# Optimization experiments

Hardware: AMD Instinct MI355X
Metric: run time of the kernel (lower is better)

## Reference

```python
import jax, jax.numpy as jnp
import numpy as np

NEG_SLOPE = 0.2  # PyG GATConv default LeakyReLU slope


def gat_layer(x, src, dst, W, a_src, a_dst, bias, num_nodes, heads, out_ch, concat):
    # x: [N, in], W: [in, heads*out_ch], a_src/a_dst: [heads, out_ch]
    h = (x @ W).reshape(num_nodes, heads, out_ch)          # [N,H,C]
    alpha_s = jnp.sum(h * a_src, axis=-1)                  # [N,H]
    alpha_d = jnp.sum(h * a_dst, axis=-1)                  # [N,H]
    e = jax.nn.leaky_relu(alpha_s[src] + alpha_d[dst], NEG_SLOPE)  # [E,H]
    # softmax over incoming edges of each destination node
    e_max = jax.ops.segment_max(e, dst, num_segments=num_nodes)   # [N,H]
    e_exp = jnp.exp(e - e_max[dst])                        # [E,H]
    denom = jax.ops.segment_sum(e_exp, dst, num_segments=num_nodes)  # [N,H]
    alpha = e_exp / denom[dst]                             # [E,H]
    msg = h[src] * alpha[:, :, None]                       # [E,H,C]
    out = jax.ops.segment_sum(msg, dst, num_segments=num_nodes)     # [N,H,C]
    if concat:
        out = out.reshape(num_nodes, heads * out_ch)
    else:
        out = out.mean(axis=1)
    return out + bias


def setup_inputs() -> dict:
    key = jax.random.key(0)
    ks = jax.random.split(key, 12)
    N, E = 50000, 800000
    IN, HID, OUT, H = 128, 32, 64, 4
    x = jax.random.normal(ks[0], (N, IN), dtype=jnp.float32)
    edge_index = jax.random.randint(ks[1], (2, E), 0, N, dtype=jnp.int32)
    s = 1.0 / np.sqrt(IN)
    W1 = jax.random.normal(ks[2], (IN, H * HID), dtype=jnp.float32) * s
    a_src1 = jax.random.normal(ks[3], (H, HID), dtype=jnp.float32) * 0.1
    a_dst1 = jax.random.normal(ks[4], (H, HID), dtype=jnp.float32) * 0.1
    b1 = jnp.zeros((H * HID,), dtype=jnp.float32)
    s2 = 1.0 / np.sqrt(H * HID)
    W2 = jax.random.normal(ks[5], (H * HID, OUT), dtype=jnp.float32) * s2
    a_src2 = jax.random.normal(ks[6], (1, OUT), dtype=jnp.float32) * 0.1
    a_dst2 = jax.random.normal(ks[7], (1, OUT), dtype=jnp.float32) * 0.1
    b2 = jnp.zeros((OUT,), dtype=jnp.float32)
    return {"x": x, "edge_index": edge_index, "W1": W1, "a_src1": a_src1,
            "a_dst1": a_dst1, "b1": b1, "W2": W2, "a_src2": a_src2,
            "a_dst2": a_dst2, "b2": b2}


def reference(x, edge_index, W1, a_src1, a_dst1, b1, W2, a_src2, a_dst2, b2):
    N = x.shape[0]
    src, dst = edge_index[0], edge_index[1]
    h = gat_layer(x, src, dst, W1, a_src1, a_dst1, b1, N, heads=4, out_ch=32, concat=True)
    h = jax.nn.elu(h)
    # dropout is identity in eval / p=0.0
    out = gat_layer(h, src, dst, W2, a_src2, a_dst2, b2, N, heads=1, out_ch=64, concat=False)
    return out
```

## Files before the change

### kernel.cpp

```cpp
#include <hip/hip_runtime.h>
#include <hip/hip_bf16.h>

#define C1 128
#define C2 64
#define CAP 96

typedef __attribute__((ext_vector_type(8))) short short8;
typedef __attribute__((ext_vector_type(4))) float floatx4;

__device__ __forceinline__ float lrelu(float v) { return v > 0.f ? v : 0.2f * v; }

__device__ __forceinline__ unsigned short f2bf(float f) {
    unsigned u = __float_as_uint(f);
    u += 0x7FFFu + ((u >> 16) & 1u);
    return (unsigned short)(u >> 16);
}

__global__ __launch_bounds__(256)
void gemm1_mfma_kernel(const float* __restrict__ x, const float* __restrict__ W1,
                       const float* __restrict__ asrc, const float* __restrict__ adst,
                       unsigned short* __restrict__ h1b,
                       float* __restrict__ as1, float* __restrict__ ad1,
                       int N) {
    __shared__ __align__(16) unsigned short Bs[128 * 136];
    for (int i = threadIdx.x; i < 128 * 64; i += 256) {
        int col = i & 127;
        int k = (i >> 7) * 2;
        unsigned w0 = f2bf(W1[k * 128 + col]);
        unsigned w1 = f2bf(W1[(k + 1) * 128 + col]);
        *(unsigned*)&Bs[col * 136 + k] = w0 | (w1 << 16);
    }
    __syncthreads();

    const int lane = threadIdx.x & 63, ww = threadIdx.x >> 6;
    const int quad = lane >> 4, l16 = lane & 15;
    const int nodeBase = blockIdx.x * 64 + ww * 16;
    int arow = nodeBase + l16;
    if (arow >= N) arow = N - 1;
    const float* xp = x + (size_t)arow * C1 + quad * 8;
    short8 afr[4];
#pragma unroll
    for (int kk = 0; kk < 4; ++kk) {
        float4 a0 = *(const float4*)(xp + kk * 32);
        float4 a1 = *(const float4*)(xp + kk * 32 + 4);
        short8 fr;
        fr[0] = (short)f2bf(a0.x); fr[1] = (short)f2bf(a0.y);
        fr[2] = (short)f2bf(a0.z); fr[3] = (short)f2bf(a0.w);
        fr[4] = (short)f2bf(a1.x); fr[5] = (short)f2bf(a1.y);
        fr[6] = (short)f2bf(a1.z); fr[7] = (short)f2bf(a1.w);
        afr[kk] = fr;
    }

    float sacc[4], dacc[4];
#pragma unroll
    for (int ct = 0; ct < 8; ++ct) {
        floatx4 acc = {0.f, 0.f, 0.f, 0.f};
        const int col = ct * 16 + l16;
        const unsigned short* bbase = &Bs[col * 136 + quad * 8];
#pragma unroll
        for (int kk = 0; kk < 4; ++kk) {
            short8 bfr = *(const short8*)(bbase + kk * 32);
            acc = __builtin_amdgcn_mfma_f32_16x16x32_bf16(afr[kk], bfr, acc, 0, 0, 0);
        }
#pragma unroll
        for (int reg = 0; reg < 4; ++reg) {
            int node = nodeBase + quad * 4 + reg;
            if (node < N) h1b[(size_t)node * C1 + col] = f2bf(acc[reg]);
        }
        float av = asrc[col];
        float dv = adst[col];
        if ((ct & 1) == 0) {
#pragma unroll
            for (int r = 0; r < 4; ++r) { sacc[r] = 0.f; dacc[r] = 0.f; }
        }
#pragma unroll
        for (int reg = 0; reg < 4; ++reg) {
            sacc[reg] += acc[reg] * av;
            dacc[reg] += acc[reg] * dv;
        }
        if ((ct & 1) == 1) {
            int h = ct >> 1;
#pragma unroll
            for (int reg = 0; reg < 4; ++reg) {
                float ts = sacc[reg], td = dacc[reg];
#pragma unroll
                for (int o = 1; o < 16; o <<= 1) {
                    ts += __shfl_xor(ts, o, 64);
                    td += __shfl_xor(td, o, 64);
                }
                if (l16 == 0) {
                    int node = nodeBase + quad * 4 + reg;
                    if (node < N) {
                        as1[node * 4 + h] = ts;
                        ad1[node * 4 + h] = td;
                    }
                }
            }
        }
    }
}

__global__ __launch_bounds__(256)
void fill_kernel(const int* __restrict__ ei, int* __restrict__ cursor,
                 int* __restrict__ csrc, int N, int E) {
    const int part = blockIdx.x & 7;
    const int bIdx = blockIdx.x >> 3;
    const int bpp  = gridDim.x >> 3;
    const int lo = (int)(((long)N * part) >> 3);
    const int hi = (int)(((long)N * (part + 1)) >> 3);

    const int E4 = ((E & 3) == 0) ? (E >> 2) : 0;
    const int4* d4 = (const int4*)(ei + E);
    const int4* s4 = (const int4*)ei;
    for (int q = bIdx * 256 + threadIdx.x; q < E4; q += bpp * 256) {
        int4 dv = d4[q];
        int4 sv = s4[q];
        int dd[4] = {dv.x, dv.y, dv.z, dv.w};
        int ss[4] = {sv.x, sv.y, sv.z, sv.w};
        int pos[4];
        bool act[4];
#pragma unroll
        for (int i = 0; i < 4; ++i) {
            act[i] = (dd[i] >= lo) & (dd[i] < hi) & ((unsigned)ss[i] < (unsigned)N);
            pos[i] = act[i] ? atomicAdd(&cursor[dd[i]], 1) : 0;
        }
#pragma unroll
        for (int i = 0; i < 4; ++i)
            if (act[i] && pos[i] < CAP) csrc[dd[i] * CAP + pos[i]] = ss[i];
    }
    for (int e = E4 * 4 + bIdx * 256 + threadIdx.x; e < E; e += bpp * 256) {
        int dd = ei[E + e];
        if (dd < lo || dd >= hi) continue;
        int ss = ei[e];
        if ((unsigned)ss >= (unsigned)N) continue;
        int pp = atomicAdd(&cursor[dd], 1);
        if (pp < CAP) csrc[dd * CAP + pp] = ss;
    }
}

__global__ __launch_bounds__(256)
void msg1_csr_kernel(const int* __restrict__ cursor, const int* __restrict__ csrc,
                     const unsigned* __restrict__ h1u, const float* __restrict__ as1,
                     const float* __restrict__ ad1, const float* __restrict__ b1,
                     float2* __restrict__ out1, int N) {
    const int d = blockIdx.x * 4 + (threadIdx.x >> 6);
    if (d >= N) return;
    const int lane = threadIdx.x & 63;
    int dg = cursor[d]; if (dg > CAP) dg = CAP;
    const int base = d * CAP;
    const int e16 = lane & 15;
    const int head = lane >> 4;
    const float wadh = ad1[d * 4 + head];
    float accx = 0.f, accy = 0.f, sumw = 0.f;
    for (int jj = 0; jj < dg; jj += 16) {
        int idx = jj + e16;
        if (idx >= dg) idx = dg - 1;
        const int myS = csrc[base + idx];
        float w = 0.f;
        if (jj + e16 < dg)
            w = __expf(lrelu(as1[myS * 4 + head] + wadh));
        unsigned rv[16];
#pragma unroll
        for (int k = 0; k < 16; ++k) {
            int s = __shfl(myS, k, 64);
            rv[k] = h1u[(unsigned)s * 64u + (unsigned)lane];
        }
#pragma unroll
        for (int k = 0; k < 16; ++k) {
            float wk = __shfl(w, (head << 4) | k, 64);
            sumw += wk;
            accx += wk * __uint_as_float(rv[k] << 16);
            accy += wk * __uint_as_float(rv[k] & 0xFFFF0000u);
        }
    }
    float inv = (sumw > 0.f) ? 1.f / sumw : 0.f;
    float rx = accx * inv + b1[2 * lane];
    float ry = accy * inv + b1[2 * lane + 1];
    rx = rx > 0.f ? rx : expm1f(rx);
    ry = ry > 0.f ? ry : expm1f(ry);
    float2 p; p.x = rx; p.y = ry;
    out1[(size_t)d * 64 + lane] = p;
}

__global__ __launch_bounds__(256)
void gemm2_mfma_kernel(const float* __restrict__ h2, const float* __restrict__ W2,
                       const float* __restrict__ asrc, const float* __restrict__ adst,
                       unsigned short* __restrict__ g2b, float* __restrict__ as2,
                       float* __restrict__ ad2, int N) {
    __shared__ __align__(16) unsigned short Bs[64 * 136];
    for (int i = threadIdx.x; i < 64 * 64; i += 256) {
        int col = i & 63;
        int k = (i >> 6) * 2;
        unsigned w0 = f2bf(W2[k * 64 + col]);
        unsigned w1 = f2bf(W2[(k + 1) * 64 + col]);
        *(unsigned*)&Bs[col * 136 + k] = w0 | (w1 << 16);
    }
    __syncthreads();

    const int lane = threadIdx.x & 63, ww = threadIdx.x >> 6;
    const int quad = lane >> 4, l16 = lane & 15;
    const int nodeBase = blockIdx.x * 64 + ww * 16;
    int arow = nodeBase + l16;
    if (arow >= N) arow = N - 1;
    const float* xp = h2 + (size_t)arow * C1 + quad * 8;
    short8 afr[4];
#pragma unroll
    for (int kk = 0; kk < 4; ++kk) {
        float4 a0 = *(const float4*)(xp + kk * 32);
        float4 a1 = *(const float4*)(xp + kk * 32 + 4);
        short8 fr;
        fr[0] = (short)f2bf(a0.x); fr[1] = (short)f2bf(a0.y);
        fr[2] = (short)f2bf(a0.z); fr[3] = (short)f2bf(a0.w);
        fr[4] = (short)f2bf(a1.x); fr[5] = (short)f2bf(a1.y);
        fr[6] = (short)f2bf(a1.z); fr[7] = (short)f2bf(a1.w);
        afr[kk] = fr;
    }

    float sacc[4] = {0.f,0.f,0.f,0.f}, dacc[4] = {0.f,0.f,0.f,0.f};
#pragma unroll
    for (int ct = 0; ct < 4; ++ct) {
        floatx4 acc = {0.f, 0.f, 0.f, 0.f};
        const int col = ct * 16 + l16;
        const unsigned short* bbase = &Bs[col * 136 + quad * 8];
#pragma unroll
        for (int kk = 0; kk < 4; ++kk) {
            short8 bfr = *(const short8*)(bbase + kk * 32);
            acc = __builtin_amdgcn_mfma_f32_16x16x32_bf16(afr[kk], bfr, acc, 0, 0, 0);
        }
#pragma unroll
        for (int reg = 0; reg < 4; ++reg) {
            int node = nodeBase + quad * 4 + reg;
            if (node < N) g2b[(size_t)node * C2 + col] = f2bf(acc[reg]);
        }
        float av = asrc[col];
        float dv = adst[col];
#pragma unroll
        for (int reg = 0; reg < 4; ++reg) {
            sacc[reg] += acc[reg] * av;
            dacc[reg] += acc[reg] * dv;
        }
    }
#pragma unroll
    for (int reg = 0; reg < 4; ++reg) {
        float ts = sacc[reg], td = dacc[reg];
#pragma unroll
        for (int o = 1; o < 16; o <<= 1) {
            ts += __shfl_xor(ts, o, 64);
            td += __shfl_xor(td, o, 64);
        }
        if (l16 == 0) {
            int node = nodeBase + quad * 4 + reg;
            if (node < N) { as2[node] = ts; ad2[node] = td; }
        }
    }
}

__global__ __launch_bounds__(256)
void msg2_csr_kernel(const int* __restrict__ cursor, const int* __restrict__ csrc,
                     const unsigned* __restrict__ g2u, const float* __restrict__ as2,
                     const float* __restrict__ ad2, const float* __restrict__ b2,
                     float2* __restrict__ y, int N) {
    const int d = blockIdx.x * 4 + (threadIdx.x >> 6);
    if (d >= N) return;
    const int lane = threadIdx.x & 63;
    const int half = lane >> 5;
    const int l32 = lane & 31;
    int dg = cursor[d]; if (dg > CAP) dg = CAP;
    const int base = d * CAP;
    const float add = ad2[d];
    float accx = 0.f, accy = 0.f, sumw = 0.f;
    for (int jj = 0; jj < dg; jj += 32) {
        int idx = jj + l32;
        if (idx >= dg) idx = dg - 1;
        const int myS = csrc[base + idx];
        float w = 0.f;
        if (lane < 32 && jj + l32 < dg)
            w = __expf(lrelu(as2[myS] + add));
        unsigned rv[16];
#pragma unroll
        for (int k = 0; k < 16; ++k) {
            int s = __shfl(myS, 2 * k + half, 64);
            rv[k] = g2u[(unsigned)s * 32u + (unsigned)l32];
        }
#pragma unroll
        for (int k = 0; k < 16; ++k) {
            float wk = __shfl(w, 2 * k + half, 64);
            sumw += wk;
            accx += wk * __uint_as_float(rv[k] << 16);
            accy += wk * __uint_as_float(rv[k] & 0xFFFF0000u);
        }
    }
    accx += __shfl_xor(accx, 32, 64);
    accy += __shfl_xor(accy, 32, 64);
    sumw += __shfl_xor(sumw, 32, 64);
    if (half == 0) {
        float inv = (sumw > 0.f) ? 1.f / sumw : 0.f;
        float2 p;
        p.x = accx * inv + b2[2 * l32];
        p.y = accy * inv + b2[2 * l32 + 1];
        y[(size_t)d * 32 + l32] = p;
    }
}

extern "C" void kernel_launch(void* const* d_in, const int* in_sizes, int n_in,
                              void* d_out, int out_size, void* d_ws, size_t ws_size,
                              hipStream_t stream) {
    const float* x    = (const float*)d_in[0];
    const int*   ei   = (const int*)d_in[1];
    const float* W1   = (const float*)d_in[2];
    const float* a_s1 = (const float*)d_in[3];
    const float* a_d1 = (const float*)d_in[4];
    const float* b1   = (const float*)d_in[5];
    const float* W2   = (const float*)d_in[6];
    const float* a_s2 = (const float*)d_in[7];
    const float* a_d2 = (const float*)d_in[8];
    const float* b2   = (const float*)d_in[9];

    const int N = in_sizes[0] / C1;
    const int E = in_sizes[1] / 2;

    auto align16 = [](size_t v) { return (v + 15) & ~(size_t)15; };
    const size_t RF   = 16;
    const size_t RCUR = align16((size_t)N * 4);
    const size_t RSRC = align16((size_t)N * CAP * 4);
    const size_t R1   = align16((size_t)N * C1 * 4);
    const size_t R2   = align16((size_t)N * 8 * 4);

    char* base = (char*)d_ws;
    int*  cursor = (int*)(base + RF);
    int*  csrc   = (int*)(base + RF + RCUR);
    char* R1p = base + RF + RCUR + RSRC;
    char* R2p = R1p + R1;
    char* R4p = R2p + R2;
    (void)ws_size;

    unsigned short* h1 = (unsigned short*)R1p;
    unsigned short* g2 = (unsigned short*)R1p;
    float* as1 = (float*)R2p;
    float* ad1 = as1 + (size_t)N * 4;
    float* as2 = (float*)R2p;
    float* ad2 = as2 + N;
    float* out1 = (float*)R4p;

    const int nbTile = (N + 63) / 64;
    const int nbWave4 = (N + 3) / 4;

    hipMemsetAsync(cursor, 0, (size_t)N * 4, stream);
    gemm1_mfma_kernel<<<nbTile, 256, 0, stream>>>(x, W1, a_s1, a_d1, h1, as1, ad1, N);
    fill_kernel<<<2048, 256, 0, stream>>>(ei, cursor, csrc, N, E);
    msg1_csr_kernel<<<nbWave4, 256, 0, stream>>>(cursor, csrc, (const unsigned*)h1,
        as1, ad1, b1, (float2*)out1, N);
    gemm2_mfma_kernel<<<nbTile, 256, 0, stream>>>(out1, W2, a_s2, a_d2, g2, as2, ad2, N);
    msg2_csr_kernel<<<nbWave4, 256, 0, stream>>>(cursor, csrc, (const unsigned*)g2,
        as2, ad2, b2, (float2*)d_out, N);
}
```

Measured before the change: 225.3 us.

## Switch to fp16 MFMA, store layer-1 output as fp16, use LDS for edge weights

Replaces the bf16 conversion and MFMA with fp16, using packed cvt_pkrtz conversions. The layer-1 output is written as packed fp16, so the second GEMM loads half the bytes and needs no conversion. The message kernels broadcast source indices with readlane or LDS and read edge weights from LDS as float4 instead of many shuffles. This cuts conversion ALU work, shuffle traffic and intermediate memory traffic. The cost is fp16 range and precision limits, and LDS round trips without explicit barriers, which relies on wave-level execution.

```diff
diff --git a/kernel.cpp b/kernel.cpp
--- a/kernel.cpp
+++ b/kernel.cpp
@@ -1,19 +1,25 @@
 #include <hip/hip_runtime.h>
-#include <hip/hip_bf16.h>
 
 #define C1 128
 #define C2 64
 #define CAP 96
 
-typedef __attribute__((ext_vector_type(8))) short short8;
+typedef __attribute__((ext_vector_type(8))) _Float16 half8;
+typedef __attribute__((ext_vector_type(2))) _Float16 half2v;
+typedef __attribute__((ext_vector_type(2))) __fp16  fp16x2;
 typedef __attribute__((ext_vector_type(4))) float floatx4;
 
 __device__ __forceinline__ float lrelu(float v) { return v > 0.f ? v : 0.2f * v; }
 
-__device__ __forceinline__ unsigned short f2bf(float f) {
-    unsigned u = __float_as_uint(f);
-    u += 0x7FFFu + ((u >> 16) & 1u);
-    return (unsigned short)(u >> 16);
+__device__ __forceinline__ unsigned short f2h(float f) {
+    union { _Float16 h; unsigned short u; } c;
+    c.h = (_Float16)f;
+    return c.u;
+}
+__device__ __forceinline__ unsigned pk2h(float a, float b) {
+    union { fp16x2 p; unsigned u; } c;
+    c.p = __builtin_amdgcn_cvt_pkrtz(a, b);
+    return c.u;
 }
 
 __global__ __launch_bounds__(256)
@@ -26,9 +32,7 @@
     for (int i = threadIdx.x; i < 128 * 64; i += 256) {
         int col = i & 127;
         int k = (i >> 7) * 2;
-        unsigned w0 = f2bf(W1[k * 128 + col]);
-        unsigned w1 = f2bf(W1[(k + 1) * 128 + col]);
-        *(unsigned*)&Bs[col * 136 + k] = w0 | (w1 << 16);
+        *(unsigned*)&Bs[col * 136 + k] = pk2h(W1[k * 128 + col], W1[(k + 1) * 128 + col]);
     }
     __syncthreads();
 
@@ -38,17 +42,17 @@
     int arow = nodeBase + l16;
     if (arow >= N) arow = N - 1;
     const float* xp = x + (size_t)arow * C1 + quad * 8;
-    short8 afr[4];
+    half8 afr[4];
 #pragma unroll
     for (int kk = 0; kk < 4; ++kk) {
         float4 a0 = *(const float4*)(xp + kk * 32);
         float4 a1 = *(const float4*)(xp + kk * 32 + 4);
-        short8 fr;
-        fr[0] = (short)f2bf(a0.x); fr[1] = (short)f2bf(a0.y);
-        fr[2] = (short)f2bf(a0.z); fr[3] = (short)f2bf(a0.w);
-        fr[4] = (short)f2bf(a1.x); fr[5] = (short)f2bf(a1.y);
-        fr[6] = (short)f2bf(a1.z); fr[7] = (short)f2bf(a1.w);
-        afr[kk] = fr;
+        union { half8 v; unsigned u[4]; } fr;
+        fr.u[0] = pk2h(a0.x, a0.y);
+        fr.u[1] = pk2h(a0.z, a0.w);
+        fr.u[2] = pk2h(a1.x, a1.y);
+        fr.u[3] = pk2h(a1.z, a1.w);
+        afr[kk] = fr.v;
     }
 
     float sacc[4], dacc[4];
@@ -59,13 +63,13 @@
         const unsigned short* bbase = &Bs[col * 136 + quad * 8];
 #pragma unroll
         for (int kk = 0; kk < 4; ++kk) {
-            short8 bfr = *(const short8*)(bbase + kk * 32);
-            acc = __builtin_amdgcn_mfma_f32_16x16x32_bf16(afr[kk], bfr, acc, 0, 0, 0);
+            half8 bfr = *(const half8*)(bbase + kk * 32);
+            acc = __builtin_amdgcn_mfma_f32_16x16x32_f16(afr[kk], bfr, acc, 0, 0, 0);
         }
 #pragma unroll
         for (int reg = 0; reg < 4; ++reg) {
             int node = nodeBase + quad * 4 + reg;
-            if (node < N) h1b[(size_t)node * C1 + col] = f2bf(acc[reg]);
+            if (node < N) h1b[(size_t)node * C1 + col] = f2h(acc[reg]);
         }
         float av = asrc[col];
         float dv = adst[col];
@@ -142,8 +146,10 @@
 void msg1_csr_kernel(const int* __restrict__ cursor, const int* __restrict__ csrc,
                      const unsigned* __restrict__ h1u, const float* __restrict__ as1,
                      const float* __restrict__ ad1, const float* __restrict__ b1,
-                     float2* __restrict__ out1, int N) {
-    const int d = blockIdx.x * 4 + (threadIdx.x >> 6);
+                     unsigned* __restrict__ out1, int N) {
+    __shared__ float ws[4][64];
+    const int wid = threadIdx.x >> 6;
+    const int d = blockIdx.x * 4 + wid;
     if (d >= N) return;
     const int lane = threadIdx.x & 63;
     int dg = cursor[d]; if (dg > CAP) dg = CAP;
@@ -156,21 +162,27 @@
         int idx = jj + e16;
         if (idx >= dg) idx = dg - 1;
         const int myS = csrc[base + idx];
+        unsigned rv[16];
+#pragma unroll
+        for (int k = 0; k < 16; ++k) {
+            int s = __builtin_amdgcn_readlane(myS, k);
+            rv[k] = h1u[(unsigned)s * 64u + (unsigned)lane];
+        }
         float w = 0.f;
         if (jj + e16 < dg)
             w = __expf(lrelu(as1[myS * 4 + head] + wadh));
-        unsigned rv[16];
-#pragma unroll
-        for (int k = 0; k < 16; ++k) {
-            int s = __shfl(myS, k, 64);
-            rv[k] = h1u[(unsigned)s * 64u + (unsigned)lane];
-        }
-#pragma unroll
-        for (int k = 0; k < 16; ++k) {
-            float wk = __shfl(w, (head << 4) | k, 64);
-            sumw += wk;
-            accx += wk * __uint_as_float(rv[k] << 16);
-            accy += wk * __uint_as_float(rv[k] & 0xFFFF0000u);
+        ws[wid][lane] = w;
+#pragma unroll
+        for (int j = 0; j < 4; ++j) {
+            float4 wf = ((const float4*)&ws[wid][head * 16])[j];
+            union { unsigned u; half2v p; } c0, c1, c2, c3;
+            c0.u = rv[4 * j + 0]; c1.u = rv[4 * j + 1];
+            c2.u = rv[4 * j + 2]; c3.u = rv[4 * j + 3];
+            sumw += (wf.x + wf.y) + (wf.z + wf.w);
+            accx += wf.x * (float)c0.p[0]; accy += wf.x * (float)c0.p[1];
+            accx += wf.y * (float)c1.p[0]; accy += wf.y * (float)c1.p[1];
+            accx += wf.z * (float)c2.p[0]; accy += wf.z * (float)c2.p[1];
+            accx += wf.w * (float)c3.p[0]; accy += wf.w * (float)c3.p[1];
         }
     }
     float inv = (sumw > 0.f) ? 1.f / sumw : 0.f;
@@ -178,12 +190,11 @@
     float ry = accy * inv + b1[2 * lane + 1];
     rx = rx > 0.f ? rx : expm1f(rx);
     ry = ry > 0.f ? ry : expm1f(ry);
-    float2 p; p.x = rx; p.y = ry;
-    out1[(size_t)d * 64 + lane] = p;
-}
-
-__global__ __launch_bounds__(256)
-void gemm2_mfma_kernel(const float* __restrict__ h2, const float* __restrict__ W2,
+    out1[(size_t)d * 64 + lane] = pk2h(rx, ry);
+}
+
+__global__ __launch_bounds__(256)
+void gemm2_mfma_kernel(const unsigned short* __restrict__ h2, const float* __restrict__ W2,
                        const float* __restrict__ asrc, const float* __restrict__ adst,
                        unsigned short* __restrict__ g2b, float* __restrict__ as2,
                        float* __restrict__ ad2, int N) {
@@ -191,9 +202,7 @@
     for (int i = threadIdx.x; i < 64 * 64; i += 256) {
         int col = i & 63;
         int k = (i >> 6) * 2;
-        unsigned w0 = f2bf(W2[k * 64 + col]);
-        unsigned w1 = f2bf(W2[(k + 1) * 64 + col]);
-        *(unsigned*)&Bs[col * 136 + k] = w0 | (w1 << 16);
+        *(unsigned*)&Bs[col * 136 + k] = pk2h(W2[k * 64 + col], W2[(k + 1) * 64 + col]);
     }
     __syncthreads();
 
@@ -202,19 +211,11 @@
     const int nodeBase = blockIdx.x * 64 + ww * 16;
     int arow = nodeBase + l16;
     if (arow >= N) arow = N - 1;
-    const float* xp = h2 + (size_t)arow * C1 + quad * 8;
-    short8 afr[4];
-#pragma unroll
-    for (int kk = 0; kk < 4; ++kk) {
-        float4 a0 = *(const float4*)(xp + kk * 32);
-        float4 a1 = *(const float4*)(xp + kk * 32 + 4);
-        short8 fr;
-        fr[0] = (short)f2bf(a0.x); fr[1] = (short)f2bf(a0.y);
-        fr[2] = (short)f2bf(a0.z); fr[3] = (short)f2bf(a0.w);
-        fr[4] = (short)f2bf(a1.x); fr[5] = (short)f2bf(a1.y);
-        fr[6] = (short)f2bf(a1.z); fr[7] = (short)f2bf(a1.w);
-        afr[kk] = fr;
-    }
+    const unsigned short* xp = h2 + (size_t)arow * C1 + quad * 8;
+    half8 afr[4];
+#pragma unroll
+    for (int kk = 0; kk < 4; ++kk)
+        afr[kk] = *(const half8*)(xp + kk * 32);
 
     float sacc[4] = {0.f,0.f,0.f,0.f}, dacc[4] = {0.f,0.f,0.f,0.f};
 #pragma unroll
@@ -224,13 +225,13 @@
         const unsigned short* bbase = &Bs[col * 136 + quad * 8];
 #pragma unroll
         for (int kk = 0; kk < 4; ++kk) {
-            short8 bfr = *(const short8*)(bbase + kk * 32);
-            acc = __builtin_amdgcn_mfma_f32_16x16x32_bf16(afr[kk], bfr, acc, 0, 0, 0);
+            half8 bfr = *(const half8*)(bbase + kk * 32);
+            acc = __builtin_amdgcn_mfma_f32_16x16x32_f16(afr[kk], bfr, acc, 0, 0, 0);
         }
 #pragma unroll
         for (int reg = 0; reg < 4; ++reg) {
             int node = nodeBase + quad * 4 + reg;
-            if (node < N) g2b[(size_t)node * C2 + col] = f2bf(acc[reg]);
+            if (node < N) g2b[(size_t)node * C2 + col] = f2h(acc[reg]);
         }
         float av = asrc[col];
         float dv = adst[col];
@@ -260,7 +261,10 @@
                      const unsigned* __restrict__ g2u, const float* __restrict__ as2,
                      const float* __restrict__ ad2, const float* __restrict__ b2,
                      float2* __restrict__ y, int N) {
-    const int d = blockIdx.x * 4 + (threadIdx.x >> 6);
+    __shared__ float wsm[4][32];
+    __shared__ int   ssm[4][32];
+    const int wid = threadIdx.x >> 6;
+    const int d = blockIdx.x * 4 + wid;
     if (d >= N) return;
     const int lane = threadIdx.x & 63;
     const int half = lane >> 5;
@@ -274,20 +278,30 @@
         if (idx >= dg) idx = dg - 1;
         const int myS = csrc[base + idx];
         float w = 0.f;
-        if (lane < 32 && jj + l32 < dg)
-            w = __expf(lrelu(as2[myS] + add));
+        if (jj + l32 < dg) w = __expf(lrelu(as2[myS] + add));
+        ssm[wid][l32] = myS;
+        wsm[wid][l32] = w;
+        int4 s0 = ((const int4*)&ssm[wid][half * 16])[0];
+        int4 s1 = ((const int4*)&ssm[wid][half * 16])[1];
+        int4 s2 = ((const int4*)&ssm[wid][half * 16])[2];
+        int4 s3 = ((const int4*)&ssm[wid][half * 16])[3];
+        int ss[16] = {s0.x, s0.y, s0.z, s0.w, s1.x, s1.y, s1.z, s1.w,
+                      s2.x, s2.y, s2.z, s2.w, s3.x, s3.y, s3.z, s3.w};
         unsigned rv[16];
 #pragma unroll
-        for (int k = 0; k < 16; ++k) {
-            int s = __shfl(myS, 2 * k + half, 64);
-            rv[k] = g2u[(unsigned)s * 32u + (unsigned)l32];
-        }
-#pragma unroll
-        for (int k = 0; k < 16; ++k) {
-            float wk = __shfl(w, 2 * k + half, 64);
-            sumw += wk;
-            accx += wk * __uint_as_float(rv[k] << 16);
-            accy += wk * __uint_as_float(rv[k] & 0xFFFF0000u);
+        for (int k = 0; k < 16; ++k)
+            rv[k] = g2u[(unsigned)ss[k] * 32u + (unsigned)l32];
+#pragma unroll
+        for (int j = 0; j < 4; ++j) {
+            float4 wf = ((const float4*)&wsm[wid][half * 16])[j];
+            union { unsigned u; half2v p; } c0, c1, c2, c3;
+            c0.u = rv[4 * j + 0]; c1.u = rv[4 * j + 1];
+            c2.u = rv[4 * j + 2]; c3.u = rv[4 * j + 3];
+            sumw += (wf.x + wf.y) + (wf.z + wf.w);
+            accx += wf.x * (float)c0.p[0]; accy += wf.x * (float)c0.p[1];
+            accx += wf.y * (float)c1.p[0]; accy += wf.y * (float)c1.p[1];
+            accx += wf.z * (float)c2.p[0]; accy += wf.z * (float)c2.p[1];
+            accx += wf.w * (float)c3.p[0]; accy += wf.w * (float)c3.p[1];
         }
     }
     accx += __shfl_xor(accx, 32, 64);
@@ -340,7 +354,7 @@
     float* ad1 = as1 + (size_t)N * 4;
     float* as2 = (float*)R2p;
     float* ad2 = as2 + N;
-    float* out1 = (float*)R4p;
+    unsigned short* out1 = (unsigned short*)R4p;
 
     const int nbTile = (N + 63) / 64;
     const int nbWave4 = (N + 3) / 4;
@@ -349,7 +363,7 @@
     gemm1_mfma_kernel<<<nbTile, 256, 0, stream>>>(x, W1, a_s1, a_d1, h1, as1, ad1, N);
     fill_kernel<<<2048, 256, 0, stream>>>(ei, cursor, csrc, N, E);
     msg1_csr_kernel<<<nbWave4, 256, 0, stream>>>(cursor, csrc, (const unsigned*)h1,
-        as1, ad1, b1, (float2*)out1, N);
+        as1, ad1, b1, (unsigned*)out1, N);
     gemm2_mfma_kernel<<<nbTile, 256, 0, stream>>>(out1, W2, a_s2, a_d2, g2, as2, ad2, N);
     msg2_csr_kernel<<<nbWave4, 256, 0, stream>>>(cursor, csrc, (const unsigned*)g2,
         as2, ad2, b2, (float2*)d_out, N);
```

Result: no change. 226.1 us (+0.3%).
